# Optimization experiments

Measured on AMD Instinct MI355X. Metric: run time of the kernel, lower is better.

Reference implementation:

```python
import jax, jax.numpy as jnp
import numpy as np

B, D, H, M, K = 128, 1024, 256, 100, 5
TAU = 0.5
EPS = 1e-5


def setup_inputs() -> dict:
    key = jax.random.key(0)
    ks = jax.random.split(key, 12)
    def w(k, i, o):
        return jax.random.normal(k, (i, o), jnp.float32) / np.sqrt(i).astype(np.float32)
    u = jax.random.uniform(ks[1], (B, M, D), jnp.float32, 1e-6, 1.0 - 1e-6)
    gumbel = -jnp.log(-jnp.log(u))  # standard Gumbel(0,1) noise
    return {
        "x": jax.random.normal(ks[0], (B, D), jnp.float32),
        "gumbel": gumbel,
        # generator: Linear(D,2H) -> LN -> ReLU -> Linear(2H,H) -> LN -> ReLU -> Linear(H, M*D)
        "gW1": w(ks[2], D, 2 * H), "gb1": jnp.zeros((2 * H,), jnp.float32),
        "ln1_s": jnp.ones((2 * H,), jnp.float32), "ln1_b": jnp.zeros((2 * H,), jnp.float32),
        "gW2": w(ks[3], 2 * H, H), "gb2": jnp.zeros((H,), jnp.float32),
        "ln2_s": jnp.ones((H,), jnp.float32), "ln2_b": jnp.zeros((H,), jnp.float32),
        "gW3": w(ks[4], H, M * D), "gb3": jnp.zeros((M * D,), jnp.float32),
        # scorer: Linear(D*K,H) -> ReLU -> Linear(H,H//2) -> ReLU -> Linear(H//2,1) -> Sigmoid
        "sW1": w(ks[5], D * K, H), "sb1": jnp.zeros((H,), jnp.float32),
        "sW2": w(ks[6], H, H // 2), "sb2": jnp.zeros((H // 2,), jnp.float32),
        "sW3": w(ks[7], H // 2, 1), "sb3": jnp.zeros((1,), jnp.float32),
        # synergy: Linear(D*K,H) -> ReLU -> Linear(H,1) -> Tanh
        "yW1": w(ks[8], D * K, H), "yb1": jnp.zeros((H,), jnp.float32),
        "yW2": w(ks[9], H, 1), "yb2": jnp.zeros((1,), jnp.float32),
    }


def _ln(h, s, b):
    mu = jnp.mean(h, axis=-1, keepdims=True)
    v = jnp.mean(jnp.square(h - mu), axis=-1, keepdims=True)
    return (h - mu) * jax.lax.rsqrt(v + EPS) * s + b


def reference(x, gumbel, gW1, gb1, ln1_s, ln1_b, gW2, gb2, ln2_s, ln2_b, gW3, gb3,
              sW1, sb1, sW2, sb2, sW3, sb3, yW1, yb1, yW2, yb2):
    Bn, Dn = x.shape
    # generator MLP (eval mode: dropout is identity)
    h = jax.nn.relu(_ln(x @ gW1 + gb1, ln1_s, ln1_b))
    h = jax.nn.relu(_ln(h @ gW2 + gb2, ln2_s, ln2_b))
    logits = (h @ gW3 + gb3).reshape(Bn, M, Dn)                      # [B,M,D]
    # gumbel-softmax (soft, eval): softmax((logits + g)/tau)
    probs = jax.nn.softmax((logits + gumbel) / TAU, axis=-1)          # [B,M,D]
    # top-k biomarker selection per combination (vectorized over B and M)
    _, idx = jax.lax.top_k(probs, K)                                  # [B,M,K] int32
    vals = jnp.take_along_axis(jnp.broadcast_to(x[:, None, :], (Bn, M, Dn)), idx, axis=-1)  # [B,M,K]
    # value-scaled one-hot layout: flat[b,m, j*D + idx_j] = x[b, idx_j]
    pos = idx + (jnp.arange(K, dtype=idx.dtype) * Dn)[None, None, :]  # [B,M,K]
    flat = jnp.zeros((Bn, M, K * Dn), x.dtype).at[
        jnp.arange(Bn)[:, None, None], jnp.arange(M)[None, :, None], pos
    ].set(vals)                                                        # [B,M,K*D] sparse one-hot values
    scores = jax.nn.sigmoid(
        jax.nn.relu(jax.nn.relu(flat @ sW1 + sb1) @ sW2 + sb2) @ sW3 + sb3
    )[..., 0]                                                          # [B,M]
    synergies = jnp.tanh(jax.nn.relu(flat @ yW1 + yb1) @ yW2 + yb2)[..., 0]  # [B,M]
    return (probs, scores, synergies, logits)
```

## Files before the change

kernel.cpp:

```cpp
#include <hip/hip_runtime.h>
#include <math.h>

#define B_   128
#define D_   1024
#define H_   256
#define M_   100
#define K_   5
#define MD   102400
#define EPS_ 1e-5f

#define OFF_SCORES 13107200
#define OFF_SYN    13120000
#define OFF_LOGITS 13132800

__device__ __forceinline__ float block_sum(float v, float* red, int t) {
  #pragma unroll
  for (int off = 1; off < 64; off <<= 1) v += __shfl_xor(v, off);
  if ((t & 63) == 0) red[t >> 6] = v;
  __syncthreads();
  float s = red[0] + red[1] + red[2] + red[3];
  __syncthreads();
  return s;
}

__device__ __forceinline__ float block_max(float v, float* red, int t) {
  #pragma unroll
  for (int off = 1; off < 64; off <<= 1) v = fmaxf(v, __shfl_xor(v, off));
  if ((t & 63) == 0) red[t >> 6] = v;
  __syncthreads();
  float s = fmaxf(fmaxf(red[0], red[1]), fmaxf(red[2], red[3]));
  __syncthreads();
  return s;
}

__device__ __forceinline__ void block_sum2(float& a, float& b, float* red, int t) {
  #pragma unroll
  for (int off = 1; off < 64; off <<= 1) { a += __shfl_xor(a, off); b += __shfl_xor(b, off); }
  if ((t & 63) == 0) { red[(t >> 6) * 2] = a; red[(t >> 6) * 2 + 1] = b; }
  __syncthreads();
  a = red[0] + red[2] + red[4] + red[6];
  b = red[1] + red[3] + red[5] + red[7];
  __syncthreads();
}

__global__ __launch_bounds__(256) void gen_mlp_kernel(
    const float* __restrict__ x,
    const float* __restrict__ gW1, const float* __restrict__ gb1,
    const float* __restrict__ ln1s, const float* __restrict__ ln1b,
    const float* __restrict__ gW2, const float* __restrict__ gb2,
    const float* __restrict__ ln2s, const float* __restrict__ ln2b,
    float* __restrict__ h2out)
{
  __shared__ float xs[1024];
  __shared__ float h1s[512];
  __shared__ float red[8];
  int b = blockIdx.x, t = threadIdx.x;
  const float* xr = x + b * 1024;
  #pragma unroll
  for (int i = 0; i < 4; ++i) xs[t + i * 256] = xr[t + i * 256];
  __syncthreads();

  float a0 = 0.f, a1 = 0.f;
  for (int d = 0; d < 1024; ++d) {
    float xv = xs[d];
    float2 w = *(const float2*)&gW1[d * 512 + 2 * t];
    a0 = fmaf(xv, w.x, a0);
    a1 = fmaf(xv, w.y, a1);
  }
  a0 += gb1[2 * t]; a1 += gb1[2 * t + 1];
  float s = a0 + a1, sq = a0 * a0 + a1 * a1;
  block_sum2(s, sq, red, t);
  float mu = s * (1.f / 512.f);
  float var = sq * (1.f / 512.f) - mu * mu;
  float inv = rsqrtf(var + EPS_);
  h1s[2 * t]     = fmaxf((a0 - mu) * inv * ln1s[2 * t]     + ln1b[2 * t],     0.f);
  h1s[2 * t + 1] = fmaxf((a1 - mu) * inv * ln1s[2 * t + 1] + ln1b[2 * t + 1], 0.f);
  __syncthreads();

  float acc = 0.f;
  for (int h = 0; h < 512; ++h) acc = fmaf(h1s[h], gW2[h * 256 + t], acc);
  acc += gb2[t];
  float s2 = acc, sq2 = acc * acc;
  block_sum2(s2, sq2, red, t);
  float mu2 = s2 * (1.f / 256.f);
  float var2 = sq2 * (1.f / 256.f) - mu2 * mu2;
  float inv2 = rsqrtf(var2 + EPS_);
  h2out[b * 256 + t] = fmaxf((acc - mu2) * inv2 * ln2s[t] + ln2b[t], 0.f);
}

__global__ __launch_bounds__(256, 3) void gemm3_kernel(
    const float* __restrict__ h2, const float* __restrict__ gW3,
    const float* __restrict__ gb3, float* __restrict__ logits)
{
  __shared__ float h2t[32 * 132];
  __shared__ float Wlds[2 * 32 * 128];
  int t = threadIdx.x;
  int lane = t & 63;
  int w = t >> 6;
  int rg8 = (t >> 4) * 8;
  int cg4 = (t & 15) * 4;
  long col0 = (long)blockIdx.x * 128;

  int bb = t >> 1;
  int ks = (t & 1) * 16;

  int krl = lane >> 5;
  int cid = (lane & 31) * 4;

  float acc[8][8];
  #pragma unroll
  for (int i = 0; i < 8; ++i)
    #pragma unroll
    for (int j = 0; j < 8; ++j) acc[i][j] = 0.f;

  #pragma unroll
  for (int p = 0; p < 4; ++p) {
    int kkrow = p * 8 + w * 2;
    const float* g = gW3 + (long)(kkrow + krl) * MD + col0 + cid;
    float* l = &Wlds[kkrow * 128];
    __builtin_amdgcn_global_load_lds(
        (const __attribute__((address_space(1))) void*)g,
        (__attribute__((address_space(3))) void*)l, 16, 0, 0);
  }
  const float* hp = &h2[bb * 256 + ks];
  float4 ha = *(const float4*)(hp + 0);
  float4 hb = *(const float4*)(hp + 4);
  float4 hc = *(const float4*)(hp + 8);
  float4 hd = *(const float4*)(hp + 12);

  #pragma unroll 1
  for (int kt = 0; kt < 8; ++kt) {
    asm volatile("s_waitcnt vmcnt(0)" ::: "memory");
    __builtin_amdgcn_s_barrier();

    {
      float vals[16] = {ha.x, ha.y, ha.z, ha.w, hb.x, hb.y, hb.z, hb.w,
                        hc.x, hc.y, hc.z, hc.w, hd.x, hd.y, hd.z, hd.w};
      #pragma unroll
      for (int j = 0; j < 16; ++j) h2t[(ks + j) * 132 + bb] = vals[j];
    }

    if (kt + 1 < 8) {
      #pragma unroll
      for (int p = 0; p < 4; ++p) {
        int kkrow = p * 8 + w * 2;
        const float* g = gW3 + ((long)(kt + 1) * 32 + kkrow + krl) * MD + col0 + cid;
        float* l = &Wlds[((kt + 1) & 1) * 4096 + kkrow * 128];
        __builtin_amdgcn_global_load_lds(
            (const __attribute__((address_space(1))) void*)g,
            (__attribute__((address_space(3))) void*)l, 16, 0, 0);
      }
      const float* hq = &h2[bb * 256 + (kt + 1) * 32 + ks];
      ha = *(const float4*)(hq + 0);
      hb = *(const float4*)(hq + 4);
      hc = *(const float4*)(hq + 8);
      hd = *(const float4*)(hq + 12);
    }

    asm volatile("s_waitcnt lgkmcnt(0)" ::: "memory");
    __builtin_amdgcn_s_barrier();

    const float* Wb = &Wlds[(kt & 1) * 4096];
    #pragma unroll 8
    for (int kk = 0; kk < 32; ++kk) {
      float4 a0 = *(const float4*)&h2t[kk * 132 + rg8];
      float4 a1 = *(const float4*)&h2t[kk * 132 + rg8 + 4];
      float4 b0 = *(const float4*)&Wb[kk * 128 + cg4];
      float4 b1 = *(const float4*)&Wb[kk * 128 + 64 + cg4];
      float a[8] = {a0.x, a0.y, a0.z, a0.w, a1.x, a1.y, a1.z, a1.w};
      float bv[8] = {b0.x, b0.y, b0.z, b0.w, b1.x, b1.y, b1.z, b1.w};
      #pragma unroll
      for (int i = 0; i < 8; ++i)
        #pragma unroll
        for (int j = 0; j < 8; ++j)
          acc[i][j] = fmaf(a[i], bv[j], acc[i][j]);
    }
  }

  float4 bias0 = *(const float4*)&gb3[col0 + cg4];
  float4 bias1 = *(const float4*)&gb3[col0 + 64 + cg4];
  #pragma unroll
  for (int i = 0; i < 8; ++i) {
    long row = rg8 + i;
    float4 o0, o1;
    o0.x = acc[i][0] + bias0.x; o0.y = acc[i][1] + bias0.y;
    o0.z = acc[i][2] + bias0.z; o0.w = acc[i][3] + bias0.w;
    o1.x = acc[i][4] + bias1.x; o1.y = acc[i][5] + bias1.y;
    o1.z = acc[i][6] + bias1.z; o1.w = acc[i][7] + bias1.w;
    *(float4*)&logits[row * MD + col0 + cg4] = o0;
    *(float4*)&logits[row * MD + col0 + 64 + cg4] = o1;
  }
}

__global__ __launch_bounds__(256) void tail_kernel(
    const float* __restrict__ x, const float* __restrict__ gumbel,
    const float* __restrict__ sW1, const float* __restrict__ sb1,
    const float* __restrict__ yW1, const float* __restrict__ yb1,
    const float* __restrict__ yW2, const float* __restrict__ yb2,
    const float* __restrict__ logits, float* __restrict__ probs,
    float* __restrict__ syn, float* __restrict__ t1ws)
{
  __shared__ float red[8];
  __shared__ float redv[4];
  __shared__ int   redi[4];
  __shared__ int   winner;
  int row = blockIdx.x;
  int t = threadIdx.x;
  int b = row / 100;
  const float* lg = logits + row * 1024;
  const float* gm = gumbel + row * 1024;

  float z[4];
  #pragma unroll
  for (int i = 0; i < 4; ++i) z[i] = (lg[t + i * 256] + gm[t + i * 256]) * 2.0f;
  float mx = fmaxf(fmaxf(z[0], z[1]), fmaxf(z[2], z[3]));
  mx = block_max(mx, red, t);
  float p[4]; float ls = 0.f;
  #pragma unroll
  for (int i = 0; i < 4; ++i) { p[i] = expf(z[i] - mx); ls += p[i]; }
  float denom = block_sum(ls, red, t);
  float inv = 1.f / denom;
  float v[4];
  #pragma unroll
  for (int i = 0; i < 4; ++i) {
    v[i] = p[i] * inv;
    probs[row * 1024 + t + i * 256] = v[i];
  }

  float t1acc = sb1[t];
  float u1acc = yb1[t];
  for (int jsel = 0; jsel < 5; ++jsel) {
    float bv = v[0]; int bi = t;
    #pragma unroll
    for (int i = 1; i < 4; ++i) {
      int idx = i * 256 + t;
      if (v[i] > bv || (v[i] == bv && idx < bi)) { bv = v[i]; bi = idx; }
    }
    #pragma unroll
    for (int off = 1; off < 64; off <<= 1) {
      float ov = __shfl_xor(bv, off);
      int oi = __shfl_xor(bi, off);
      if (ov > bv || (ov == bv && oi < bi)) { bv = ov; bi = oi; }
    }
    if ((t & 63) == 0) { redv[t >> 6] = bv; redi[t >> 6] = bi; }
    __syncthreads();
    if (t == 0) {
      float wv = redv[0]; int wi = redi[0];
      #pragma unroll
      for (int w = 1; w < 4; ++w)
        if (redv[w] > wv || (redv[w] == wv && redi[w] < wi)) { wv = redv[w]; wi = redi[w]; }
      winner = wi;
    }
    __syncthreads();
    int w = winner;
    if ((w & 255) == t) v[w >> 8] = -1.f;
    float xv = x[b * 1024 + w];
    t1acc = fmaf(xv, sW1[(jsel * 1024 + w) * 256 + t], t1acc);
    u1acc = fmaf(xv, yW1[(jsel * 1024 + w) * 256 + t], u1acc);
    __syncthreads();
  }

  float t1v = fmaxf(t1acc, 0.f);
  float u1v = fmaxf(u1acc, 0.f);
  t1ws[row * 256 + t] = t1v;

  float part = u1v * yW2[t];
  float dsum = block_sum(part, red, t);
  if (t == 0) syn[row] = tanhf(dsum + yb2[0]);
}

__global__ __launch_bounds__(256) void scorer2_kernel(
    const float* __restrict__ t1, const float* __restrict__ sW2,
    const float* __restrict__ sb2, const float* __restrict__ sW3,
    const float* __restrict__ sb3, float* __restrict__ scores)
{
  __shared__ float t1t[64 * 68];
  __shared__ float red[64 * 32];
  int t = threadIdx.x;
  int row0 = blockIdx.x * 64;
  int c4 = (t & 31) * 4;
  int r8 = (t >> 5) * 8;
  float acc[8][4];
  #pragma unroll
  for (int i = 0; i < 8; ++i)
    #pragma unroll
    for (int j = 0; j < 4; ++j) acc[i][j] = 0.f;

  for (int c = 0; c < 4; ++c) {
    #pragma unroll
    for (int p = 0; p < 16; ++p) {
      int rr = p * 4 + (t >> 6);
      int kk = t & 63;
      t1t[kk * 68 + rr] = t1[(row0 + rr) * 256 + c * 64 + kk];
    }
    __syncthreads();
    #pragma unroll 4
    for (int kk = 0; kk < 64; ++kk) {
      float4 bf = *(const float4*)&sW2[(c * 64 + kk) * 128 + c4];
      float4 a0 = *(const float4*)&t1t[kk * 68 + r8];
      float4 a1 = *(const float4*)&t1t[kk * 68 + r8 + 4];
      float a[8] = {a0.x, a0.y, a0.z, a0.w, a1.x, a1.y, a1.z, a1.w};
      float bv[4] = {bf.x, bf.y, bf.z, bf.w};
      #pragma unroll
      for (int i = 0; i < 8; ++i)
        #pragma unroll
        for (int j = 0; j < 4; ++j) acc[i][j] = fmaf(a[i], bv[j], acc[i][j]);
    }
    __syncthreads();
  }

  float4 b2 = *(const float4*)&sb2[c4];
  float4 w3 = *(const float4*)&sW3[c4];
  #pragma unroll
  for (int i = 0; i < 8; ++i) {
    float s = fmaxf(acc[i][0] + b2.x, 0.f) * w3.x
            + fmaxf(acc[i][1] + b2.y, 0.f) * w3.y
            + fmaxf(acc[i][2] + b2.z, 0.f) * w3.z
            + fmaxf(acc[i][3] + b2.w, 0.f) * w3.w;
    red[(r8 + i) * 32 + (t & 31)] = s;
  }
  __syncthreads();
  if (t < 64) {
    float s = sb3[0];
    #pragma unroll
    for (int g = 0; g < 32; ++g) s += red[t * 32 + g];
    scores[row0 + t] = 1.f / (1.f + expf(-s));
  }
}

extern "C" void kernel_launch(void* const* d_in, const int* in_sizes, int n_in,
                              void* d_out, int out_size, void* d_ws, size_t ws_size,
                              hipStream_t stream) {
  const float* x    = (const float*)d_in[0];
  const float* gum  = (const float*)d_in[1];
  const float* gW1  = (const float*)d_in[2];
  const float* gb1  = (const float*)d_in[3];
  const float* ln1s = (const float*)d_in[4];
  const float* ln1b = (const float*)d_in[5];
  const float* gW2  = (const float*)d_in[6];
  const float* gb2  = (const float*)d_in[7];
  const float* ln2s = (const float*)d_in[8];
  const float* ln2b = (const float*)d_in[9];
  const float* gW3  = (const float*)d_in[10];
  const float* gb3  = (const float*)d_in[11];
  const float* sW1  = (const float*)d_in[12];
  const float* sb1  = (const float*)d_in[13];
  const float* sW2  = (const float*)d_in[14];
  const float* sb2  = (const float*)d_in[15];
  const float* sW3  = (const float*)d_in[16];
  const float* sb3  = (const float*)d_in[17];
  const float* yW1  = (const float*)d_in[18];
  const float* yb1  = (const float*)d_in[19];
  const float* yW2  = (const float*)d_in[20];
  const float* yb2  = (const float*)d_in[21];

  float* out    = (float*)d_out;
  float* probs  = out;
  float* scores = out + OFF_SCORES;
  float* syn    = out + OFF_SYN;
  float* logits = out + OFF_LOGITS;

  float* h2 = (float*)d_ws;
  float* t1 = (float*)((char*)d_ws + 131072 * 4);

  gen_mlp_kernel<<<128, 256, 0, stream>>>(x, gW1, gb1, ln1s, ln1b, gW2, gb2, ln2s, ln2b, h2);
  gemm3_kernel<<<800, 256, 0, stream>>>(h2, gW3, gb3, logits);
  tail_kernel<<<12800, 256, 0, stream>>>(x, gum, sW1, sb1, yW1, yb1, yW2, yb2,
                                         logits, probs, syn, t1);
  scorer2_kernel<<<200, 256, 0, stream>>>(t1, sW2, sb2, sW3, sb3, scores);
}
```

Baseline: 466.3 us.

## Triple-buffer gemm3 W tiles and batch tail top-k selection per wave

```diff
diff --git a/kernel.cpp b/kernel.cpp
--- a/kernel.cpp
+++ b/kernel.cpp
@@ -88,21 +88,21 @@
   h2out[b * 256 + t] = fmaxf((acc - mu2) * inv2 * ln2s[t] + ln2b[t], 0.f);
 }
 
-__global__ __launch_bounds__(256, 3) void gemm3_kernel(
+__global__ __launch_bounds__(256, 4) void gemm3_kernel(
     const float* __restrict__ h2, const float* __restrict__ gW3,
     const float* __restrict__ gb3, float* __restrict__ logits)
 {
-  __shared__ float h2t[32 * 132];
-  __shared__ float Wlds[2 * 32 * 128];
+  __shared__ float h2t[16 * 132];
+  __shared__ float Wlds[3 * 16 * 128];
   int t = threadIdx.x;
   int lane = t & 63;
-  int w = t >> 6;
+  int wv = t >> 6;
   int rg8 = (t >> 4) * 8;
   int cg4 = (t & 15) * 4;
   long col0 = (long)blockIdx.x * 128;
 
   int bb = t >> 1;
-  int ks = (t & 1) * 16;
+  int ks = (t & 1) * 8;
 
   int krl = lane >> 5;
   int cid = (lane & 31) * 4;
@@ -113,69 +113,74 @@
     #pragma unroll
     for (int j = 0; j < 8; ++j) acc[i][j] = 0.f;
 
-  #pragma unroll
-  for (int p = 0; p < 4; ++p) {
-    int kkrow = p * 8 + w * 2;
-    const float* g = gW3 + (long)(kkrow + krl) * MD + col0 + cid;
-    float* l = &Wlds[kkrow * 128];
-    __builtin_amdgcn_global_load_lds(
-        (const __attribute__((address_space(1))) void*)g,
-        (__attribute__((address_space(3))) void*)l, 16, 0, 0);
-  }
-  const float* hp = &h2[bb * 256 + ks];
-  float4 ha = *(const float4*)(hp + 0);
-  float4 hb = *(const float4*)(hp + 4);
-  float4 hc = *(const float4*)(hp + 8);
-  float4 hd = *(const float4*)(hp + 12);
+#define ISSUE_W(kt_, s_)                                                           \
+  {                                                                                \
+    int c0_ = wv * 2;                                                              \
+    const float* g0_ = gW3 + ((long)(kt_) * 16 + 2 * c0_ + krl) * MD + col0 + cid; \
+    float* l0_ = &Wlds[(s_) * 2048 + c0_ * 256];                                   \
+    __builtin_amdgcn_global_load_lds(                                              \
+        (const __attribute__((address_space(1))) void*)g0_,                        \
+        (__attribute__((address_space(3))) void*)l0_, 16, 0, 0);                   \
+    int c1_ = wv * 2 + 1;                                                          \
+    const float* g1_ = gW3 + ((long)(kt_) * 16 + 2 * c1_ + krl) * MD + col0 + cid; \
+    float* l1_ = &Wlds[(s_) * 2048 + c1_ * 256];                                   \
+    __builtin_amdgcn_global_load_lds(                                              \
+        (const __attribute__((address_space(1))) void*)g1_,                        \
+        (__attribute__((address_space(3))) void*)l1_, 16, 0, 0);                   \
+  }
+
+  ISSUE_W(0, 0);
+  asm volatile("" ::: "memory");
+  const float* hp0 = &h2[bb * 256 + ks];
+  float4 ha = *(const float4*)(hp0);
+  float4 hb = *(const float4*)(hp0 + 4);
+  asm volatile("" ::: "memory");
+  ISSUE_W(1, 1);
 
   #pragma unroll 1
-  for (int kt = 0; kt < 8; ++kt) {
-    asm volatile("s_waitcnt vmcnt(0)" ::: "memory");
+  for (int kt = 0; kt < 16; ++kt) {
+    if (kt == 15) { asm volatile("s_waitcnt vmcnt(0)" ::: "memory"); }
+    else         { asm volatile("s_waitcnt vmcnt(2)" ::: "memory"); }
     __builtin_amdgcn_s_barrier();
 
-    {
-      float vals[16] = {ha.x, ha.y, ha.z, ha.w, hb.x, hb.y, hb.z, hb.w,
-                        hc.x, hc.y, hc.z, hc.w, hd.x, hd.y, hd.z, hd.w};
-      #pragma unroll
-      for (int j = 0; j < 16; ++j) h2t[(ks + j) * 132 + bb] = vals[j];
-    }
-
-    if (kt + 1 < 8) {
-      #pragma unroll
-      for (int p = 0; p < 4; ++p) {
-        int kkrow = p * 8 + w * 2;
-        const float* g = gW3 + ((long)(kt + 1) * 32 + kkrow + krl) * MD + col0 + cid;
-        float* l = &Wlds[((kt + 1) & 1) * 4096 + kkrow * 128];
-        __builtin_amdgcn_global_load_lds(
-            (const __attribute__((address_space(1))) void*)g,
-            (__attribute__((address_space(3))) void*)l, 16, 0, 0);
-      }
-      const float* hq = &h2[bb * 256 + (kt + 1) * 32 + ks];
-      ha = *(const float4*)(hq + 0);
+    h2t[(ks + 0) * 132 + bb] = ha.x;
+    h2t[(ks + 1) * 132 + bb] = ha.y;
+    h2t[(ks + 2) * 132 + bb] = ha.z;
+    h2t[(ks + 3) * 132 + bb] = ha.w;
+    h2t[(ks + 4) * 132 + bb] = hb.x;
+    h2t[(ks + 5) * 132 + bb] = hb.y;
+    h2t[(ks + 6) * 132 + bb] = hb.z;
+    h2t[(ks + 7) * 132 + bb] = hb.w;
+
+    asm volatile("" ::: "memory");
+    if (kt < 15) {
+      const float* hq = &h2[bb * 256 + (kt + 1) * 16 + ks];
+      ha = *(const float4*)(hq);
       hb = *(const float4*)(hq + 4);
-      hc = *(const float4*)(hq + 8);
-      hd = *(const float4*)(hq + 12);
-    }
+    }
+    asm volatile("" ::: "memory");
+    if (kt < 14) ISSUE_W(kt + 2, (kt + 2) % 3);
 
     asm volatile("s_waitcnt lgkmcnt(0)" ::: "memory");
     __builtin_amdgcn_s_barrier();
 
-    const float* Wb = &Wlds[(kt & 1) * 4096];
-    #pragma unroll 8
-    for (int kk = 0; kk < 32; ++kk) {
+    const float* Wb = &Wlds[(kt % 3) * 2048];
+    #pragma unroll
+    for (int kk = 0; kk < 16; ++kk) {
       float4 a0 = *(const float4*)&h2t[kk * 132 + rg8];
       float4 a1 = *(const float4*)&h2t[kk * 132 + rg8 + 4];
       float4 b0 = *(const float4*)&Wb[kk * 128 + cg4];
       float4 b1 = *(const float4*)&Wb[kk * 128 + 64 + cg4];
       float a[8] = {a0.x, a0.y, a0.z, a0.w, a1.x, a1.y, a1.z, a1.w};
-      float bv[8] = {b0.x, b0.y, b0.z, b0.w, b1.x, b1.y, b1.z, b1.w};
+      float bvv[8] = {b0.x, b0.y, b0.z, b0.w, b1.x, b1.y, b1.z, b1.w};
       #pragma unroll
       for (int i = 0; i < 8; ++i)
         #pragma unroll
         for (int j = 0; j < 8; ++j)
-          acc[i][j] = fmaf(a[i], bv[j], acc[i][j]);
-    }
-  }
+          acc[i][j] = fmaf(a[i], bvv[j], acc[i][j]);
+    }
+  }
+#undef ISSUE_W
 
   float4 bias0 = *(const float4*)&gb3[col0 + cg4];
   float4 bias1 = *(const float4*)&gb3[col0 + 64 + cg4];
@@ -201,9 +206,9 @@
     float* __restrict__ syn, float* __restrict__ t1ws)
 {
   __shared__ float red[8];
-  __shared__ float redv[4];
-  __shared__ int   redi[4];
-  __shared__ int   winner;
+  __shared__ float candV[20];
+  __shared__ int   candI[20];
+  __shared__ int   wsel[5];
   int row = blockIdx.x;
   int t = threadIdx.x;
   int b = row / 100;
@@ -227,8 +232,8 @@
     probs[row * 1024 + t + i * 256] = v[i];
   }
 
-  float t1acc = sb1[t];
-  float u1acc = yb1[t];
+  int wid = t >> 6;
+  #pragma unroll
   for (int jsel = 0; jsel < 5; ++jsel) {
     float bv = v[0]; int bi = t;
     #pragma unroll
@@ -242,23 +247,56 @@
       int oi = __shfl_xor(bi, off);
       if (ov > bv || (ov == bv && oi < bi)) { bv = ov; bi = oi; }
     }
-    if ((t & 63) == 0) { redv[t >> 6] = bv; redi[t >> 6] = bi; }
-    __syncthreads();
-    if (t == 0) {
-      float wv = redv[0]; int wi = redi[0];
+    if ((t & 63) == 0) { candV[wid * 5 + jsel] = bv; candI[wid * 5 + jsel] = bi; }
+    #pragma unroll
+    for (int i = 0; i < 4; ++i)
+      if (bi == i * 256 + t) v[i] = -1.f;
+  }
+  __syncthreads();
+
+  if (t < 64) {
+    float cV[20]; int cI[20];
+    #pragma unroll
+    for (int i = 0; i < 20; ++i) { cV[i] = candV[i]; cI[i] = candI[i]; }
+    float pv = 2.0f; int pi = -1;
+    int w0 = 0, w1 = 0, w2 = 0, w3 = 0, w4 = 0;
+    #pragma unroll
+    for (int jsel = 0; jsel < 5; ++jsel) {
+      float bv = -1.0f; int bi = 0x7FFFFFFF;
       #pragma unroll
-      for (int w = 1; w < 4; ++w)
-        if (redv[w] > wv || (redv[w] == wv && redi[w] < wi)) { wv = redv[w]; wi = redi[w]; }
-      winner = wi;
-    }
-    __syncthreads();
-    int w = winner;
-    if ((w & 255) == t) v[w >> 8] = -1.f;
-    float xv = x[b * 1024 + w];
-    t1acc = fmaf(xv, sW1[(jsel * 1024 + w) * 256 + t], t1acc);
-    u1acc = fmaf(xv, yW1[(jsel * 1024 + w) * 256 + t], u1acc);
-    __syncthreads();
-  }
+      for (int i = 0; i < 20; ++i) {
+        bool ltp = (cV[i] < pv) || (cV[i] == pv && cI[i] > pi);
+        bool gtc = (cV[i] > bv) || (cV[i] == bv && cI[i] < bi);
+        if (ltp && gtc) { bv = cV[i]; bi = cI[i]; }
+      }
+      if      (jsel == 0) w0 = bi;
+      else if (jsel == 1) w1 = bi;
+      else if (jsel == 2) w2 = bi;
+      else if (jsel == 3) w3 = bi;
+      else                w4 = bi;
+      pv = bv; pi = bi;
+    }
+    if (t == 0) { wsel[0] = w0; wsel[1] = w1; wsel[2] = w2; wsel[3] = w3; wsel[4] = w4; }
+  }
+  __syncthreads();
+
+  int ws0 = wsel[0], ws1 = wsel[1], ws2 = wsel[2], ws3 = wsel[3], ws4 = wsel[4];
+  const float* xb = x + b * 1024;
+  float x0 = xb[ws0], x1 = xb[ws1], x2 = xb[ws2], x3 = xb[ws3], x4 = xb[ws4];
+
+  float t1acc = sb1[t];
+  t1acc = fmaf(x0, sW1[(0 * 1024 + ws0) * 256 + t], t1acc);
+  t1acc = fmaf(x1, sW1[(1 * 1024 + ws1) * 256 + t], t1acc);
+  t1acc = fmaf(x2, sW1[(2 * 1024 + ws2) * 256 + t], t1acc);
+  t1acc = fmaf(x3, sW1[(3 * 1024 + ws3) * 256 + t], t1acc);
+  t1acc = fmaf(x4, sW1[(4 * 1024 + ws4) * 256 + t], t1acc);
+
+  float u1acc = yb1[t];
+  u1acc = fmaf(x0, yW1[(0 * 1024 + ws0) * 256 + t], u1acc);
+  u1acc = fmaf(x1, yW1[(1 * 1024 + ws1) * 256 + t], u1acc);
+  u1acc = fmaf(x2, yW1[(2 * 1024 + ws2) * 256 + t], u1acc);
+  u1acc = fmaf(x3, yW1[(3 * 1024 + ws3) * 256 + t], u1acc);
+  u1acc = fmaf(x4, yW1[(4 * 1024 + ws4) * 256 + t], u1acc);
 
   float t1v = fmaxf(t1acc, 0.f);
   float u1v = fmaxf(u1acc, 0.f);
```

After: 637.1 us. 36.6% more time.

## Process one softmax/top-k row per wavefront instead of per block

Applied to the files above, without the earlier changes.

```diff
diff --git a/kernel.cpp b/kernel.cpp
--- a/kernel.cpp
+++ b/kernel.cpp
@@ -19,16 +19,6 @@
   if ((t & 63) == 0) red[t >> 6] = v;
   __syncthreads();
   float s = red[0] + red[1] + red[2] + red[3];
-  __syncthreads();
-  return s;
-}
-
-__device__ __forceinline__ float block_max(float v, float* red, int t) {
-  #pragma unroll
-  for (int off = 1; off < 64; off <<= 1) v = fmaxf(v, __shfl_xor(v, off));
-  if ((t & 63) == 0) red[t >> 6] = v;
-  __syncthreads();
-  float s = fmaxf(fmaxf(red[0], red[1]), fmaxf(red[2], red[3]));
   __syncthreads();
   return s;
 }
@@ -200,41 +190,67 @@
     const float* __restrict__ logits, float* __restrict__ probs,
     float* __restrict__ syn, float* __restrict__ t1ws)
 {
-  __shared__ float red[8];
-  __shared__ float redv[4];
-  __shared__ int   redi[4];
-  __shared__ int   winner;
-  int row = blockIdx.x;
   int t = threadIdx.x;
+  int lane = t & 63;
+  int wid = t >> 6;
+  int row = blockIdx.x * 4 + wid;
   int b = row / 100;
+  int c4 = lane * 4;
   const float* lg = logits + row * 1024;
   const float* gm = gumbel + row * 1024;
 
-  float z[4];
-  #pragma unroll
-  for (int i = 0; i < 4; ++i) z[i] = (lg[t + i * 256] + gm[t + i * 256]) * 2.0f;
-  float mx = fmaxf(fmaxf(z[0], z[1]), fmaxf(z[2], z[3]));
-  mx = block_max(mx, red, t);
-  float p[4]; float ls = 0.f;
-  #pragma unroll
-  for (int i = 0; i < 4; ++i) { p[i] = expf(z[i] - mx); ls += p[i]; }
-  float denom = block_sum(ls, red, t);
-  float inv = 1.f / denom;
-  float v[4];
+  float4 v[4];
   #pragma unroll
   for (int i = 0; i < 4; ++i) {
-    v[i] = p[i] * inv;
-    probs[row * 1024 + t + i * 256] = v[i];
-  }
-
-  float t1acc = sb1[t];
-  float u1acc = yb1[t];
+    float4 a = *(const float4*)&lg[i * 256 + c4];
+    float4 g = *(const float4*)&gm[i * 256 + c4];
+    v[i].x = (a.x + g.x) * 2.0f;
+    v[i].y = (a.y + g.y) * 2.0f;
+    v[i].z = (a.z + g.z) * 2.0f;
+    v[i].w = (a.w + g.w) * 2.0f;
+  }
+
+  float mx = v[0].x;
+  #pragma unroll
+  for (int i = 0; i < 4; ++i) {
+    mx = fmaxf(mx, fmaxf(fmaxf(v[i].x, v[i].y), fmaxf(v[i].z, v[i].w)));
+  }
+  #pragma unroll
+  for (int off = 1; off < 64; off <<= 1) mx = fmaxf(mx, __shfl_xor(mx, off));
+
+  float ls = 0.f;
+  #pragma unroll
+  for (int i = 0; i < 4; ++i) {
+    v[i].x = expf(v[i].x - mx); ls += v[i].x;
+    v[i].y = expf(v[i].y - mx); ls += v[i].y;
+    v[i].z = expf(v[i].z - mx); ls += v[i].z;
+    v[i].w = expf(v[i].w - mx); ls += v[i].w;
+  }
+  #pragma unroll
+  for (int off = 1; off < 64; off <<= 1) ls += __shfl_xor(ls, off);
+  float inv = 1.f / ls;
+
+  #pragma unroll
+  for (int i = 0; i < 4; ++i) {
+    v[i].x *= inv; v[i].y *= inv; v[i].z *= inv; v[i].w *= inv;
+    *(float4*)&probs[row * 1024 + i * 256 + c4] = v[i];
+  }
+
+  const float* xb = x + b * 1024;
+  float4 t1a = *(const float4*)&sb1[c4 & 255];
+  float4 u1a = *(const float4*)&yb1[c4];
+
+  #pragma unroll
   for (int jsel = 0; jsel < 5; ++jsel) {
-    float bv = v[0]; int bi = t;
-    #pragma unroll
-    for (int i = 1; i < 4; ++i) {
-      int idx = i * 256 + t;
-      if (v[i] > bv || (v[i] == bv && idx < bi)) { bv = v[i]; bi = idx; }
+    float bv = v[0].x; int bi = 0 * 256 + c4 + 0;
+    #pragma unroll
+    for (int i = 0; i < 4; ++i) {
+      float cv[4] = {v[i].x, v[i].y, v[i].z, v[i].w};
+      #pragma unroll
+      for (int j = 0; j < 4; ++j) {
+        int idx = i * 256 + c4 + j;
+        if (cv[j] > bv || (cv[j] == bv && idx < bi)) { bv = cv[j]; bi = idx; }
+      }
     }
     #pragma unroll
     for (int off = 1; off < 64; off <<= 1) {
@@ -242,31 +258,39 @@
       int oi = __shfl_xor(bi, off);
       if (ov > bv || (ov == bv && oi < bi)) { bv = ov; bi = oi; }
     }
-    if ((t & 63) == 0) { redv[t >> 6] = bv; redi[t >> 6] = bi; }
-    __syncthreads();
-    if (t == 0) {
-      float wv = redv[0]; int wi = redi[0];
-      #pragma unroll
-      for (int w = 1; w < 4; ++w)
-        if (redv[w] > wv || (redv[w] == wv && redi[w] < wi)) { wv = redv[w]; wi = redi[w]; }
-      winner = wi;
-    }
-    __syncthreads();
-    int w = winner;
-    if ((w & 255) == t) v[w >> 8] = -1.f;
-    float xv = x[b * 1024 + w];
-    t1acc = fmaf(xv, sW1[(jsel * 1024 + w) * 256 + t], t1acc);
-    u1acc = fmaf(xv, yW1[(jsel * 1024 + w) * 256 + t], u1acc);
-    __syncthreads();
-  }
-
-  float t1v = fmaxf(t1acc, 0.f);
-  float u1v = fmaxf(u1acc, 0.f);
-  t1ws[row * 256 + t] = t1v;
-
-  float part = u1v * yW2[t];
-  float dsum = block_sum(part, red, t);
-  if (t == 0) syn[row] = tanhf(dsum + yb2[0]);
+    int wi = bi;
+
+    #pragma unroll
+    for (int i = 0; i < 4; ++i) {
+      if (wi == i * 256 + c4 + 0) v[i].x = -1.f;
+      if (wi == i * 256 + c4 + 1) v[i].y = -1.f;
+      if (wi == i * 256 + c4 + 2) v[i].z = -1.f;
+      if (wi == i * 256 + c4 + 3) v[i].w = -1.f;
+    }
+
+    float xv = xb[wi];
+    float4 sw = *(const float4*)&sW1[(jsel * 1024 + wi) * 256 + c4];
+    float4 yw = *(const float4*)&yW1[(jsel * 1024 + wi) * 256 + c4];
+    t1a.x = fmaf(xv, sw.x, t1a.x); t1a.y = fmaf(xv, sw.y, t1a.y);
+    t1a.z = fmaf(xv, sw.z, t1a.z); t1a.w = fmaf(xv, sw.w, t1a.w);
+    u1a.x = fmaf(xv, yw.x, u1a.x); u1a.y = fmaf(xv, yw.y, u1a.y);
+    u1a.z = fmaf(xv, yw.z, u1a.z); u1a.w = fmaf(xv, yw.w, u1a.w);
+  }
+
+  float4 t1v;
+  t1v.x = fmaxf(t1a.x, 0.f); t1v.y = fmaxf(t1a.y, 0.f);
+  t1v.z = fmaxf(t1a.z, 0.f); t1v.w = fmaxf(t1a.w, 0.f);
+  *(float4*)&t1ws[row * 256 + c4] = t1v;
+
+  float4 u1v;
+  u1v.x = fmaxf(u1a.x, 0.f); u1v.y = fmaxf(u1a.y, 0.f);
+  u1v.z = fmaxf(u1a.z, 0.f); u1v.w = fmaxf(u1a.w, 0.f);
+
+  float4 w2 = *(const float4*)&yW2[c4];
+  float part = u1v.x * w2.x + u1v.y * w2.y + u1v.z * w2.z + u1v.w * w2.w;
+  #pragma unroll
+  for (int off = 1; off < 64; off <<= 1) part += __shfl_xor(part, off);
+  if (lane == 0) syn[row] = tanhf(part + yb2[0]);
 }
 
 __global__ __launch_bounds__(256) void scorer2_kernel(
@@ -365,7 +389,7 @@
 
   gen_mlp_kernel<<<128, 256, 0, stream>>>(x, gW1, gb1, ln1s, ln1b, gW2, gb2, ln2s, ln2b, h2);
   gemm3_kernel<<<800, 256, 0, stream>>>(h2, gW3, gb3, logits);
-  tail_kernel<<<12800, 256, 0, stream>>>(x, gum, sW1, sb1, yW1, yb1, yW2, yb2,
-                                         logits, probs, syn, t1);
+  tail_kernel<<<3200, 256, 0, stream>>>(x, gum, sW1, sb1, yW1, yb1, yW2, yb2,
+                                        logits, probs, syn, t1);
   scorer2_kernel<<<200, 256, 0, stream>>>(t1, sW2, sb2, sW3, sb3, scores);
 }
```

After: 448.6 us. 3.8% less time.
